# Kernel tuning notes

Hardware: AMD Instinct MI355X
Metric: run time of the kernel (lower is better)

Reference implementation:

```python
import jax, jax.numpy as jnp
import numpy as np

B, W, KD, NC, D, NN, NH, AD, HOPS = 512, 4, 64, 32, 256, 16, 8, 32, 4
DH = D // NH
DFF = 4 * D
P = B * W + B
ROLE_WRITER, ROLE_QUERY = 0, 1


def setup_inputs() -> dict:
    key = jax.random.key(0)
    ks = iter(jax.random.split(key, 40))
    f = lambda shape, s=0.02: jax.random.normal(next(ks), shape, dtype=jnp.float32) * s
    inp = {
        'query_keys': jax.random.normal(next(ks), (B, KD), dtype=jnp.float32),
        'writer_keys': jax.random.normal(next(ks), (B, W, KD), dtype=jnp.float32),
        'key_proj_w': f((KD, D)), 'key_proj_b': jnp.zeros((D,), jnp.float32),
        'class_embed': f((NC, D)), 'role_embed': f((3, D)), 'start_node_embed': f((NN, D)),
        'input_ln_g': jnp.ones((D,), jnp.float32), 'input_ln_b': jnp.zeros((D,), jnp.float32),
        'ln1_g': jnp.ones((NN, D), jnp.float32), 'ln1_b': jnp.zeros((NN, D), jnp.float32),
        'wqkv': f((NN, D, 3 * D)), 'bqkv': jnp.zeros((NN, 3 * D), jnp.float32),
        'wo': f((NN, D, D)), 'bo': jnp.zeros((NN, D), jnp.float32),
        'ln2_g': jnp.ones((NN, D), jnp.float32), 'ln2_b': jnp.zeros((NN, D), jnp.float32),
        'w_fc1': f((NN, D, DFF)), 'b_fc1': jnp.zeros((NN, DFF), jnp.float32),
        'w_fc2': f((NN, DFF, D)), 'b_fc2': jnp.zeros((NN, D), jnp.float32),
        'delta_w': jnp.zeros((D, D), jnp.float32), 'delta_b': jnp.zeros((D,), jnp.float32),
        'dir_w': f((D, D)), 'dir_b': jnp.zeros((D,), jnp.float32),
        'mag_w': f((D, 1)), 'mag_b': jnp.full((1,), 2.5, jnp.float32),
        'out_w': f((D, NC)), 'out_b': jnp.zeros((NC,), jnp.float32),
        'address_table': jax.random.normal(next(ks), (NN, AD), dtype=jnp.float32),
        'query_start_nodes': jax.random.randint(next(ks), (B,), 0, NN),
        'writer_labels': jax.random.randint(next(ks), (B, W), 0, NC),
        'writer_start_nodes': jax.random.randint(next(ks), (B, W), 0, NN),
    }
    return inp


def _ln(x):
    m = jnp.mean(x, -1, keepdims=True)
    v = jnp.var(x, -1, keepdims=True)
    return (x - m) * jax.lax.rsqrt(v + 1e-5)


def _forward(query_keys, writer_keys, key_proj_w, key_proj_b, class_embed, role_embed,
             start_node_embed, input_ln_g, input_ln_b, ln1_g, ln1_b, wqkv, bqkv, wo, bo,
             ln2_g, ln2_b, w_fc1, b_fc1, w_fc2, b_fc2, delta_w, delta_b, dir_w, dir_b,
             mag_w, mag_b, out_w, out_b, address_table,
             query_start_nodes, writer_labels, writer_start_nodes):
    # ---- encode writers (encode_writers) ----
    fk = writer_keys.reshape(-1, KD)          # [B*W, KD]
    fl = writer_labels.reshape(-1)            # [B*W]
    fs = writer_start_nodes.reshape(-1)       # [B*W]
    learned_w = fk @ key_proj_w + key_proj_b + class_embed[fl] + start_node_embed[fs] + role_embed[ROLE_WRITER]
    sw = jnp.zeros_like(learned_w).at[:, :KD].set(fk)
    sw = sw.at[:, KD:KD + NC].set(jax.nn.one_hot(fl, NC, dtype=learned_w.dtype))
    enc_w = _ln(learned_w) * input_ln_g + input_ln_b + sw
    # ---- encode queries (encode_queries) ----
    learned_q = query_keys @ key_proj_w + key_proj_b + start_node_embed[query_start_nodes] + role_embed[ROLE_QUERY]
    sq = jnp.zeros_like(learned_q).at[:, :KD].set(query_keys)
    enc_q = _ln(learned_q) * input_ln_g + input_ln_b + sq

    h = jnp.concatenate([enc_w, enc_q], axis=0)          # [P, D]
    node = jnp.concatenate([fs, query_start_nodes], 0)   # [P] current compute node per packet

    inv_sqrt_dh = 1.0 / np.sqrt(DH).astype(np.float32)
    for _ in range(HOPS):
        oh = jax.nn.one_hot(node, NN, dtype=h.dtype)      # [P, NN] dispatch weights

        def pnl(x, Wn, bn):
            # per-node linear: gather-compute-scatter via MoE-style dense dispatch
            xe = jnp.einsum('pn,pd->npd', oh, x)          # [NN, P, din]
            ye = jnp.einsum('npd,ndf->npf', xe, Wn)       # [NN, P, dout]
            return jnp.einsum('npf,pn->pf', ye, oh) + oh @ bn

        # ComputeNodeCell: pre-LN attention among packets at the same node
        x = _ln(h) * (oh @ ln1_g) + oh @ ln1_b
        qkv = pnl(x, wqkv, bqkv)                          # [P, 3D]
        q, k, v = jnp.split(qkv, 3, axis=-1)
        q = q.reshape(P, NH, DH); k = k.reshape(P, NH, DH); v = v.reshape(P, NH, DH)
        scores = jnp.einsum('phd,qhd->hpq', q, k) * inv_sqrt_dh   # [NH, P, P]
        same = node[:, None] == node[None, :]
        scores = jnp.where(same[None], scores, -1e9)
        attn = jax.nn.softmax(scores, axis=-1)
        ao = jnp.einsum('hpq,qhd->phd', attn, v).reshape(P, D)
        h = h + pnl(ao, wo, bo)
        # MLP block
        x2 = _ln(h) * (oh @ ln2_g) + oh @ ln2_b
        h = h + pnl(jax.nn.gelu(pnl(x2, w_fc1, b_fc1)), w_fc2, b_fc2)
        # routing heads: pick next node from address table, apply gated delta
        direction = h @ dir_w + dir_b
        node = jnp.argmax(direction[:, :AD] @ address_table.T, axis=-1)
        h = h + (h @ delta_w + delta_b) * jax.nn.sigmoid(h @ mag_w + mag_b)

    return h @ out_w + out_b                              # [P, NC] per-packet logits


def reference(query_keys, writer_keys, key_proj_w, key_proj_b, class_embed, role_embed,
              start_node_embed, input_ln_g, input_ln_b, ln1_g, ln1_b, wqkv, bqkv, wo, bo,
              ln2_g, ln2_b, w_fc1, b_fc1, w_fc2, b_fc2, delta_w, delta_b, dir_w, dir_b,
              mag_w, mag_b, out_w, out_b, address_table,
              query_start_nodes, writer_labels, writer_start_nodes):
    return _forward(query_keys, writer_keys, key_proj_w, key_proj_b, class_embed, role_embed,
                    start_node_embed, input_ln_g, input_ln_b, ln1_g, ln1_b, wqkv, bqkv, wo, bo,
                    ln2_g, ln2_b, w_fc1, b_fc1, w_fc2, b_fc2, delta_w, delta_b, dir_w, dir_b,
                    mag_w, mag_b, out_w, out_b, address_table,
                    query_start_nodes, writer_labels, writer_start_nodes)
```

## Files before the change

kernel.cpp:

```cpp
#include <hip/hip_runtime.h>
#include <math.h>

#define B_    512
#define W_    4
#define KD_   64
#define NC_   32
#define D_    256
#define NN_   16
#define NH_   8
#define AD_   32
#define HOPS_ 4
#define DH_   32
#define DFF_  1024
#define P_    2560
#define BW_   2048
#define MAXT_ 56

#define INV_SQRT_DH 0.17677669529663687f

__device__ __forceinline__ float block_sum256(float v, float* red) {
#pragma unroll
  for (int off = 32; off > 0; off >>= 1) v += __shfl_xor(v, off, 64);
  int wid = threadIdx.x >> 6;
  if ((threadIdx.x & 63) == 0) red[wid] = v;
  __syncthreads();
  float s = red[0] + red[1] + red[2] + red[3];
  __syncthreads();
  return s;
}

__device__ __forceinline__ float gelu_tanh(float v) {
  float u = 0.7978845608028654f * (v + 0.044715f * v * v * v);
  return 0.5f * v * (1.0f + tanhf(u));
}

__global__ __launch_bounds__(256) void encode_kernel(
    const float* __restrict__ query_keys, const float* __restrict__ writer_keys,
    const float* __restrict__ kpw, const float* __restrict__ kpb,
    const float* __restrict__ ce, const float* __restrict__ re,
    const float* __restrict__ sne, const float* __restrict__ ilg,
    const float* __restrict__ ilb, const int* __restrict__ qsn,
    const int* __restrict__ wl, const int* __restrict__ wsn,
    float* __restrict__ h, int* __restrict__ node) {
  int p = blockIdx.x, t = threadIdx.x;
  __shared__ float fk[KD_];
  __shared__ float red[4];
  const float* key;
  int lab = -1, sn, role;
  if (p < BW_) { key = writer_keys + (size_t)p * KD_; lab = wl[p]; sn = wsn[p]; role = 0; }
  else { int b = p - BW_; key = query_keys + (size_t)b * KD_; sn = qsn[b]; role = 1; }
  if (t < KD_) fk[t] = key[t];
  __syncthreads();

  float acc = kpb[t] + sne[sn * D_ + t] + re[role * D_ + t];
  if (lab >= 0) acc += ce[lab * D_ + t];
#pragma unroll 8
  for (int i = 0; i < KD_; i++) acc += fk[i] * kpw[i * D_ + t];

  float mean = block_sum256(acc, red) * (1.0f / D_);
  float d = acc - mean;
  float var = block_sum256(d * d, red) * (1.0f / D_);
  float xn = d * (1.0f / sqrtf(var + 1e-5f));

  float sw = 0.0f;
  if (t < KD_) sw = fk[t];
  else if (lab >= 0 && t < KD_ + NC_) sw = (t - KD_ == lab) ? 1.0f : 0.0f;

  h[(size_t)p * D_ + t] = xn * ilg[t] + ilb[t] + sw;
  if (t == 0) node[p] = sn;
}

__global__ __launch_bounds__(256) void sort_kernel(const int* __restrict__ node,
                                                   int* __restrict__ order,
                                                   int* __restrict__ invord,
                                                   int* __restrict__ offs,
                                                   int* __restrict__ cnts,
                                                   int* __restrict__ tnode,
                                                   int* __restrict__ tstart,
                                                   int* __restrict__ tend,
                                                   int* __restrict__ ntiles) {
  __shared__ int c[NN_], o[NN_], cur[NN_];
  int t = threadIdx.x;
  if (t < NN_) c[t] = 0;
  __syncthreads();
  for (int p = t; p < P_; p += 256) atomicAdd(&c[node[p]], 1);
  __syncthreads();
  if (t == 0) {
    int s = 0;
    for (int n = 0; n < NN_; n++) { o[n] = s; cur[n] = s; s += c[n]; }
    int idx = 0;
    for (int n = 0; n < NN_; n++) {
      int e = o[n] + c[n];
      for (int m0 = o[n]; m0 < e; m0 += 64) {
        tnode[idx] = n; tstart[idx] = m0; tend[idx] = e; idx++;
      }
    }
    ntiles[0] = idx;
  }
  __syncthreads();
  if (t < NN_) { cnts[t] = c[t]; offs[t] = o[t]; }
  for (int p = t; p < P_; p += 256) {
    int r = atomicAdd(&cur[node[p]], 1);
    order[r] = p;
    invord[p] = r;
  }
}

__global__ __launch_bounds__(256) void ln_affine(const float* __restrict__ h,
                                                 const float* __restrict__ g,
                                                 const float* __restrict__ b,
                                                 const int* __restrict__ node,
                                                 const int* __restrict__ order,
                                                 float* __restrict__ x) {
  int sp = blockIdx.x, t = threadIdx.x;
  __shared__ float red[4];
  int p = order[sp];
  int n = node[p];
  float v = h[(size_t)p * D_ + t];
  float mean = block_sum256(v, red) * (1.0f / D_);
  float d = v - mean;
  float var = block_sum256(d * d, red) * (1.0f / D_);
  float xn = d * (1.0f / sqrtf(var + 1e-5f));
  x[(size_t)sp * D_ + t] = xn * g[n * D_ + t] + b[n * D_ + t];
}

template <int DIN, int DOUT, int JT, int ACT, int RESID, int PER_NODE, int KSPLIT, int ADDP>
__global__ __launch_bounds__(256) void glin(const float* __restrict__ x,
                                            const float* __restrict__ W,
                                            const float* __restrict__ bias,
                                            float* __restrict__ out,
                                            float* __restrict__ pbuf,
                                            const int* __restrict__ order,
                                            const int* __restrict__ invord,
                                            const int* __restrict__ tnode,
                                            const int* __restrict__ tstart,
                                            const int* __restrict__ tend,
                                            const int* __restrict__ ntiles) {
  constexpr int KC = 32, STX = 68;
  constexpr int CPT = JT / 16;
  constexpr int HALF = 64;
  constexpr int KLEN = DIN / KSPLIT;
  constexpr int NCH = KLEN / KC;
  constexpr int LPR = JT / 4;
  constexpr int RPI = 64 / LPR;

  int ti = blockIdx.x;
  int n, s0, s1;
  if (PER_NODE) {
    if (ti >= ntiles[0]) return;
    n = tnode[ti]; s0 = tstart[ti]; s1 = tend[ti];
  } else {
    n = 0; s0 = ti * 64; s1 = P_;
  }
  int jbase = blockIdx.y * JT;
  int kz = (KSPLIT > 1) ? blockIdx.z : 0;
  int k0 = kz * KLEN;
  int rows = s1 - s0; if (rows > 64) rows = 64;

  __shared__ float xs[2][KC][STX];
  __shared__ float ws[2][KC][JT];

  int tid = threadIdx.x;
  const float* Wn = W + (size_t)n * DIN * DOUT + jbase;

  int xrow = tid >> 2, xq = tid & 3;
  bool xvalid = xrow < rows;
  const float* xptr = x + (size_t)(s0 + (xvalid ? xrow : 0)) * DIN + k0 + xq * 4;
  const float* pptr = nullptr;
  if (ADDP) {
    int pr = xvalid ? invord[s0 + xrow] : 0;
    pptr = pbuf + (size_t)pr * DIN + k0 + xq * 4;
  }

  float4 xr0, xr1;
  auto xfetch = [&](int kc) {
    if (xvalid) {
      xr0 = *(const float4*)(xptr + kc);
      xr1 = *(const float4*)(xptr + kc + 16);
      if (ADDP) {
        float4 p0 = *(const float4*)(pptr + kc);
        float4 p1 = *(const float4*)(pptr + kc + 16);
        xr0.x += p0.x; xr0.y += p0.y; xr0.z += p0.z; xr0.w += p0.w;
        xr1.x += p1.x; xr1.y += p1.y; xr1.z += p1.z; xr1.w += p1.w;
      }
    } else {
      xr0 = make_float4(0.f, 0.f, 0.f, 0.f);
      xr1 = make_float4(0.f, 0.f, 0.f, 0.f);
    }
  };
  auto xstage = [&](int buf) {
    xs[buf][xq * 4 + 0][xrow] = xr0.x;
    xs[buf][xq * 4 + 1][xrow] = xr0.y;
    xs[buf][xq * 4 + 2][xrow] = xr0.z;
    xs[buf][xq * 4 + 3][xrow] = xr0.w;
    xs[buf][xq * 4 + 16][xrow] = xr1.x;
    xs[buf][xq * 4 + 17][xrow] = xr1.y;
    xs[buf][xq * 4 + 18][xrow] = xr1.z;
    xs[buf][xq * 4 + 19][xrow] = xr1.w;
  };
  int wvw = tid >> 6, lane = tid & 63;
  int wlr = lane / LPR;
  int wlc = (lane % LPR) * 4;
  auto wfetch = [&](int buf, int kc) {
#pragma unroll
    for (int i = 0; i < 8 / RPI; i++) {
      int kr = wvw * 8 + i * RPI;
      const float* g = &Wn[(size_t)(k0 + kc + kr + wlr) * DOUT + wlc];
      __builtin_amdgcn_global_load_lds(
          (const __attribute__((address_space(1))) unsigned int*)g,
          (__attribute__((address_space(3))) unsigned int*)&ws[buf][kr][0],
          16, 0, 0);
    }
  };

  wfetch(0, 0);
  xfetch(0);
  xstage(0);
  __syncthreads();

  int r4 = (tid >> 4) * 4;
  int jc4 = (tid & 15) * 4;
  float acc[4][CPT];
#pragma unroll
  for (int r = 0; r < 4; r++)
#pragma unroll
    for (int cc = 0; cc < CPT; cc++) acc[r][cc] = 0.f;

  for (int c = 0; c < NCH; c++) {
    int cur = c & 1;
    if (c + 1 < NCH) {
      wfetch(cur ^ 1, (c + 1) * KC);
      xfetch((c + 1) * KC);
    }
#pragma unroll 8
    for (int k = 0; k < KC; k++) {
      float4 a = *(const float4*)&xs[cur][k][r4];
      float av[4] = {a.x, a.y, a.z, a.w};
      float bv[CPT];
      float4 b0 = *(const float4*)&ws[cur][k][jc4];
      bv[0] = b0.x; bv[1] = b0.y; bv[2] = b0.z; bv[3] = b0.w;
      if (CPT == 8) {
        float4 b1 = *(const float4*)&ws[cur][k][jc4 + HALF];
        bv[4] = b1.x; bv[5] = b1.y; bv[6] = b1.z; bv[7] = b1.w;
      }
#pragma unroll
      for (int r = 0; r < 4; r++)
#pragma unroll
        for (int cc = 0; cc < CPT; cc++) acc[r][cc] += av[r] * bv[cc];
    }
    if (c + 1 < NCH) xstage(cur ^ 1);
    __syncthreads();
  }

  bool main_part = (KSPLIT == 1) || (kz == 0);
  float bbv[CPT];
#pragma unroll
  for (int cc = 0; cc < 4; cc++) bbv[cc] = bias[n * DOUT + jbase + jc4 + cc];
  if (CPT == 8) {
#pragma unroll
    for (int cc = 0; cc < 4; cc++) bbv[4 + cc] = bias[n * DOUT + jbase + jc4 + HALF + cc];
  }

#pragma unroll
  for (int r = 0; r < 4; r++) {
    int lr = r4 + r;
    if (lr >= rows) continue;
    float v[CPT];
    if (main_part) {
#pragma unroll
      for (int cc = 0; cc < CPT; cc++) {
        v[cc] = acc[r][cc] + bbv[cc];
        if (ACT == 1) v[cc] = gelu_tanh(v[cc]);
      }
      if (RESID) {
        int pp = PER_NODE ? order[s0 + lr] : (s0 + lr);
        float* op = &out[(size_t)pp * DOUT + jbase + jc4];
        {
          float4 old = *(const float4*)op;
          *(float4*)op = make_float4(v[0] + old.x, v[1] + old.y, v[2] + old.z, v[3] + old.w);
        }
        if (CPT == 8) {
          float4 old = *(const float4*)(op + HALF);
          *(float4*)(op + HALF) =
              make_float4(v[4] + old.x, v[5] + old.y, v[6] + old.z, v[7] + old.w);
        }
      } else {
        float* op = &out[(size_t)(s0 + lr) * DOUT + jbase + jc4];
        *(float4*)op = make_float4(v[0], v[1], v[2], v[3]);
        if (CPT == 8)
          *(float4*)(op + HALF) = make_float4(v[4], v[5], v[6], v[7]);
      }
    } else {
      float* op = &pbuf[(size_t)(s0 + lr) * DOUT + jbase + jc4];
      *(float4*)op = make_float4(acc[r][0], acc[r][1], acc[r][2], acc[r][3]);
      if (CPT == 8)
        *(float4*)(op + HALF) = make_float4(acc[r][4], acc[r][5], acc[r][6], acc[r][7]);
    }
  }
}

#define ATS 36
__global__ __launch_bounds__(256) void attn_kernel(const float* __restrict__ qkv,
                                                   const int* __restrict__ node,
                                                   const int* __restrict__ order,
                                                   const int* __restrict__ offs,
                                                   const int* __restrict__ cnts,
                                                   float* __restrict__ ao) {
  __shared__ float qs[32 * ATS];
  __shared__ float kts[32 * ATS];
  __shared__ float vs[32 * ATS];
  __shared__ float ps[32 * ATS];
  __shared__ int glo[32], ghi[32];

  int t = threadIdx.x;
  int r = t >> 3;
  int j4 = (t & 7) * 4;
  int r0 = blockIdx.x * 32;
  int hd = blockIdx.y;

  if (t < 32) {
    int n = node[order[r0 + t]];
    glo[t] = offs[n];
    ghi[t] = offs[n] + cnts[n];
  }
  __syncthreads();

  {
    const float* qp = &qkv[(size_t)(r0 + r) * 768 + hd * 32 + j4];
    float4 q4 = *(const float4*)qp;
    q4.x *= INV_SQRT_DH; q4.y *= INV_SQRT_DH; q4.z *= INV_SQRT_DH; q4.w *= INV_SQRT_DH;
    *(float4*)&qs[r * ATS + j4] = q4;
  }

  int lo = glo[0];
  int hi = ghi[31];
  int myglo = glo[r], myghi = ghi[r];

  float4 o4 = {0.f, 0.f, 0.f, 0.f};
  float mrow = -1e30f, lrow = 0.f;

  for (int kt = lo; kt < hi; kt += 32) {
    int sj = kt + r;
    float4 k4 = {0.f, 0.f, 0.f, 0.f}, v4 = {0.f, 0.f, 0.f, 0.f};
    if (sj < hi) {
      const float* kp = &qkv[(size_t)sj * 768 + 256 + hd * 32 + j4];
      k4 = *(const float4*)kp;
      v4 = *(const float4*)(kp + 256);
    }
    __syncthreads();
    kts[(j4 + 0) * ATS + r] = k4.x;
    kts[(j4 + 1) * ATS + r] = k4.y;
    kts[(j4 + 2) * ATS + r] = k4.z;
    kts[(j4 + 3) * ATS + r] = k4.w;
    *(float4*)&vs[r * ATS + j4] = v4;
    __syncthreads();

    float s0 = 0.f, s1 = 0.f, s2 = 0.f, s3 = 0.f;
#pragma unroll 8
    for (int d = 0; d < 32; d++) {
      float qv = qs[r * ATS + d];
      float4 kv = *(const float4*)&kts[d * ATS + j4];
      s0 += qv * kv.x; s1 += qv * kv.y; s2 += qv * kv.z; s3 += qv * kv.w;
    }
    int c0 = kt + j4;
    if (c0 + 0 < myglo || c0 + 0 >= myghi) s0 = -1e30f;
    if (c0 + 1 < myglo || c0 + 1 >= myghi) s1 = -1e30f;
    if (c0 + 2 < myglo || c0 + 2 >= myghi) s2 = -1e30f;
    if (c0 + 3 < myglo || c0 + 3 >= myghi) s3 = -1e30f;

    float mx = fmaxf(fmaxf(s0, s1), fmaxf(s2, s3));
#pragma unroll
    for (int off = 4; off > 0; off >>= 1) mx = fmaxf(mx, __shfl_xor(mx, off, 8));
    float mnew = fmaxf(mrow, mx);
    float alpha = __expf(mrow - mnew);
    float p0 = __expf(s0 - mnew), p1 = __expf(s1 - mnew);
    float p2 = __expf(s2 - mnew), p3 = __expf(s3 - mnew);
    float ls = p0 + p1 + p2 + p3;
#pragma unroll
    for (int off = 4; off > 0; off >>= 1) ls += __shfl_xor(ls, off, 8);
    lrow = lrow * alpha + ls;
    mrow = mnew;
    o4.x *= alpha; o4.y *= alpha; o4.z *= alpha; o4.w *= alpha;

    *(float4*)&ps[r * ATS + j4] = make_float4(p0, p1, p2, p3);
#pragma unroll 8
    for (int j = 0; j < 32; j++) {
      float pj = ps[r * ATS + j];
      float4 vv = *(const float4*)&vs[j * ATS + j4];
      o4.x += pj * vv.x; o4.y += pj * vv.y; o4.z += pj * vv.z; o4.w += pj * vv.w;
    }
  }

  float inv = 1.f / lrow;
  o4.x *= inv; o4.y *= inv; o4.z *= inv; o4.w *= inv;
  *(float4*)&ao[(size_t)(r0 + r) * D_ + hd * 32 + j4] = o4;
}

__global__ __launch_bounds__(256) void route_kernel(float* __restrict__ h,
                                                    const float* __restrict__ pbuf,
                                                    const int* __restrict__ invord,
                                                    const float* __restrict__ dir_w,
                                                    const float* __restrict__ dir_b,
                                                    const float* __restrict__ at,
                                                    const float* __restrict__ mag_w,
                                                    const float* __restrict__ mag_b,
                                                    const float* __restrict__ delta,
                                                    int* __restrict__ node) {
  int p = blockIdx.x, t = threadIdx.x;
  __shared__ float hs[D_];
  __shared__ float dpart[8][AD_];
  __shared__ float dirs[AD_];
  __shared__ float scs[NN_];
  __shared__ float red[4];
  float hv = h[(size_t)p * D_ + t] + pbuf[(size_t)invord[p] * D_ + t];
  hs[t] = hv;
  __syncthreads();

  int j = t & 31, seg = t >> 5;
  float part = 0.0f;
#pragma unroll 8
  for (int i = 0; i < 32; i++) {
    int ii = seg * 32 + i;
    part += hs[ii] * dir_w[ii * D_ + j];
  }
  dpart[seg][j] = part;
  __syncthreads();
  if (t < AD_) {
    float s = dir_b[t];
#pragma unroll
    for (int g = 0; g < 8; g++) s += dpart[g][t];
    dirs[t] = s;
  }
  __syncthreads();
  if (t < NN_) {
    float s = 0.0f;
#pragma unroll
    for (int a = 0; a < AD_; a++) s += dirs[a] * at[t * AD_ + a];
    scs[t] = s;
  }
  __syncthreads();
  if (t == 0) {
    float best = scs[0];
    int arg = 0;
    for (int nn = 1; nn < NN_; nn++)
      if (scs[nn] > best) { best = scs[nn]; arg = nn; }
    node[p] = arg;
  }
  float mag = block_sum256(hv * mag_w[t], red) + mag_b[0];
  float sig = 1.0f / (1.0f + __expf(-mag));
  h[(size_t)p * D_ + t] = hv + delta[(size_t)p * D_ + t] * sig;
}

__global__ __launch_bounds__(256) void out_kernel(const float* __restrict__ h,
                                                  const float* __restrict__ ow,
                                                  const float* __restrict__ ob,
                                                  float* __restrict__ out) {
  int p = blockIdx.x, t = threadIdx.x;
  __shared__ float hs[D_];
  __shared__ float part[8][NC_];
  hs[t] = h[(size_t)p * D_ + t];
  __syncthreads();
  int j = t & 31, seg = t >> 5;
  float s = 0.0f;
#pragma unroll 8
  for (int i = 0; i < 32; i++) {
    int ii = seg * 32 + i;
    s += hs[ii] * ow[ii * NC_ + j];
  }
  part[seg][j] = s;
  __syncthreads();
  if (t < NC_) {
    float r = ob[t];
#pragma unroll
    for (int g = 0; g < 8; g++) r += part[g][t];
    out[(size_t)p * NC_ + t] = r;
  }
}

extern "C" void kernel_launch(void* const* d_in, const int* in_sizes, int n_in,
                              void* d_out, int out_size, void* d_ws, size_t ws_size,
                              hipStream_t stream) {
  (void)in_sizes; (void)n_in; (void)out_size; (void)ws_size;
  const float* query_keys       = (const float*)d_in[0];
  const float* writer_keys      = (const float*)d_in[1];
  const float* key_proj_w       = (const float*)d_in[2];
  const float* key_proj_b       = (const float*)d_in[3];
  const float* class_embed      = (const float*)d_in[4];
  const float* role_embed       = (const float*)d_in[5];
  const float* start_node_embed = (const float*)d_in[6];
  const float* input_ln_g       = (const float*)d_in[7];
  const float* input_ln_b       = (const float*)d_in[8];
  const float* ln1_g            = (const float*)d_in[9];
  const float* ln1_b            = (const float*)d_in[10];
  const float* wqkv             = (const float*)d_in[11];
  const float* bqkv             = (const float*)d_in[12];
  const float* wo               = (const float*)d_in[13];
  const float* bo               = (const float*)d_in[14];
  const float* ln2_g            = (const float*)d_in[15];
  const float* ln2_b            = (const float*)d_in[16];
  const float* w_fc1            = (const float*)d_in[17];
  const float* b_fc1            = (const float*)d_in[18];
  const float* w_fc2            = (const float*)d_in[19];
  const float* b_fc2            = (const float*)d_in[20];
  const float* delta_w          = (const float*)d_in[21];
  const float* delta_b          = (const float*)d_in[22];
  const float* dir_w            = (const float*)d_in[23];
  const float* dir_b            = (const float*)d_in[24];
  const float* mag_w            = (const float*)d_in[25];
  const float* mag_b            = (const float*)d_in[26];
  const float* out_w            = (const float*)d_in[27];
  const float* out_b            = (const float*)d_in[28];
  const float* address_table    = (const float*)d_in[29];
  const int* query_start_nodes  = (const int*)d_in[30];
  const int* writer_labels      = (const int*)d_in[31];
  const int* writer_start_nodes = (const int*)d_in[32];

  uintptr_t basep = (uintptr_t)d_ws;
  auto carve = [&](size_t bytes) {
    basep = (basep + 255) & ~(uintptr_t)255;
    void* r = (void*)basep;
    basep += bytes;
    return r;
  };
  float* h    = (float*)carve((size_t)P_ * D_ * 4);
  float* x    = (float*)carve((size_t)P_ * D_ * 4);
  float* qkvb = (float*)carve((size_t)P_ * 3 * D_ * 4);
  float* ff   = (float*)carve((size_t)P_ * DFF_ * 4);
  float* pbuf = (float*)carve((size_t)P_ * D_ * 4);
  int* node   = (int*)carve(P_ * 4);
  int* order  = (int*)carve(P_ * 4);
  int* invord = (int*)carve(P_ * 4);
  int* offs   = (int*)carve(NN_ * 4);
  int* cnts   = (int*)carve(NN_ * 4);
  int* tnode  = (int*)carve(MAXT_ * 4);
  int* tstart = (int*)carve(MAXT_ * 4);
  int* tend   = (int*)carve(MAXT_ * 4);
  int* ntiles = (int*)carve(4);

  encode_kernel<<<P_, 256, 0, stream>>>(query_keys, writer_keys, key_proj_w, key_proj_b,
                                        class_embed, role_embed, start_node_embed,
                                        input_ln_g, input_ln_b, query_start_nodes,
                                        writer_labels, writer_start_nodes, h, node);

  for (int hop = 0; hop < HOPS_; ++hop) {
    sort_kernel<<<1, 256, 0, stream>>>(node, order, invord, offs, cnts,
                                       tnode, tstart, tend, ntiles);
    ln_affine<<<P_, 256, 0, stream>>>(h, ln1_g, ln1_b, node, order, x);
    glin<256, 768, 128, 0, 0, 1, 1, 0><<<dim3(MAXT_, 6), 256, 0, stream>>>(
        x, wqkv, bqkv, qkvb, nullptr, order, invord, tnode, tstart, tend, ntiles);
    attn_kernel<<<dim3(P_ / 32, NH_), 256, 0, stream>>>(qkvb, node, order, offs, cnts,
                                                        x );
    glin<256, 256, 64, 0, 1, 1, 1, 0><<<dim3(MAXT_, 4), 256, 0, stream>>>(
        x, wo, bo, h, nullptr, order, invord, tnode, tstart, tend, ntiles);
    ln_affine<<<P_, 256, 0, stream>>>(h, ln2_g, ln2_b, node, order, x);
    glin<256, 1024, 128, 1, 0, 1, 1, 0><<<dim3(MAXT_, 8), 256, 0, stream>>>(
        x, w_fc1, b_fc1, ff, nullptr, order, invord, tnode, tstart, tend, ntiles);
    glin<1024, 256, 128, 0, 1, 1, 2, 0><<<dim3(MAXT_, 2, 2), 256, 0, stream>>>(
        ff, w_fc2, b_fc2, h, pbuf, order, invord, tnode, tstart, tend, ntiles);
    glin<256, 256, 64, 0, 0, 0, 1, 1><<<dim3(P_ / 64, 4), 256, 0, stream>>>(
        h, delta_w, delta_b, qkvb , pbuf, order, invord,
        tnode, tstart, tend, ntiles);
    route_kernel<<<P_, 256, 0, stream>>>(h, pbuf, invord, dir_w, dir_b, address_table,
                                         mag_w, mag_b, qkvb, node);
  }

  out_kernel<<<P_, 256, 0, stream>>>(h, out_w, out_b, (float*)d_out);
}
```

Before: 962.8 us.

## Split-K the QKV and FC1 GEMMs, folding partial sums into consumers

The QKV and FC1 projections now use a two-way K split, which doubles their grid. The two partial outputs go to separate buffers. Attention sums the two QKV partials when it loads Q/K/V, and the FC2 kernel sums the two FC1 partials and applies GELU in its input fetch. This adds parallelism to under-occupied per-node GEMMs, at the cost of extra partial-buffer traffic and GELU being recomputed per output column tile.

```diff
diff --git a/kernel.cpp b/kernel.cpp
--- a/kernel.cpp
+++ b/kernel.cpp
@@ -124,12 +124,13 @@
   x[(size_t)sp * D_ + t] = xn * g[n * D_ + t] + b[n * D_ + t];
 }
 
-template <int DIN, int DOUT, int JT, int ACT, int RESID, int PER_NODE, int KSPLIT, int ADDP>
+template <int DIN, int DOUT, int JT, int ACT, int RESID, int PER_NODE, int KSPLIT, int XMODE>
 __global__ __launch_bounds__(256) void glin(const float* __restrict__ x,
                                             const float* __restrict__ W,
                                             const float* __restrict__ bias,
                                             float* __restrict__ out,
                                             float* __restrict__ pbuf,
+                                            const float* __restrict__ xaux,
                                             const int* __restrict__ order,
                                             const int* __restrict__ invord,
                                             const int* __restrict__ tnode,
@@ -166,10 +167,12 @@
   int xrow = tid >> 2, xq = tid & 3;
   bool xvalid = xrow < rows;
   const float* xptr = x + (size_t)(s0 + (xvalid ? xrow : 0)) * DIN + k0 + xq * 4;
-  const float* pptr = nullptr;
-  if (ADDP) {
+  const float* aptr = nullptr;
+  if (XMODE == 1) {
     int pr = xvalid ? invord[s0 + xrow] : 0;
-    pptr = pbuf + (size_t)pr * DIN + k0 + xq * 4;
+    aptr = xaux + (size_t)pr * DIN + k0 + xq * 4;
+  } else if (XMODE == 2) {
+    aptr = xaux + (size_t)(s0 + (xvalid ? xrow : 0)) * DIN + k0 + xq * 4;
   }
 
   float4 xr0, xr1;
@@ -177,11 +180,17 @@
     if (xvalid) {
       xr0 = *(const float4*)(xptr + kc);
       xr1 = *(const float4*)(xptr + kc + 16);
-      if (ADDP) {
-        float4 p0 = *(const float4*)(pptr + kc);
-        float4 p1 = *(const float4*)(pptr + kc + 16);
+      if (XMODE != 0) {
+        float4 p0 = *(const float4*)(aptr + kc);
+        float4 p1 = *(const float4*)(aptr + kc + 16);
         xr0.x += p0.x; xr0.y += p0.y; xr0.z += p0.z; xr0.w += p0.w;
         xr1.x += p1.x; xr1.y += p1.y; xr1.z += p1.z; xr1.w += p1.w;
+        if (XMODE == 2) {
+          xr0.x = gelu_tanh(xr0.x); xr0.y = gelu_tanh(xr0.y);
+          xr0.z = gelu_tanh(xr0.z); xr0.w = gelu_tanh(xr0.w);
+          xr1.x = gelu_tanh(xr1.x); xr1.y = gelu_tanh(xr1.y);
+          xr1.z = gelu_tanh(xr1.z); xr1.w = gelu_tanh(xr1.w);
+        }
       }
     } else {
       xr0 = make_float4(0.f, 0.f, 0.f, 0.f);
@@ -301,6 +310,7 @@
 
 #define ATS 36
 __global__ __launch_bounds__(256) void attn_kernel(const float* __restrict__ qkv,
+                                                   const float* __restrict__ qkvp,
                                                    const int* __restrict__ node,
                                                    const int* __restrict__ order,
                                                    const int* __restrict__ offs,
@@ -326,9 +336,13 @@
   __syncthreads();
 
   {
-    const float* qp = &qkv[(size_t)(r0 + r) * 768 + hd * 32 + j4];
-    float4 q4 = *(const float4*)qp;
-    q4.x *= INV_SQRT_DH; q4.y *= INV_SQRT_DH; q4.z *= INV_SQRT_DH; q4.w *= INV_SQRT_DH;
+    size_t off = (size_t)(r0 + r) * 768 + hd * 32 + j4;
+    float4 q4 = *(const float4*)&qkv[off];
+    float4 qp = *(const float4*)&qkvp[off];
+    q4.x = (q4.x + qp.x) * INV_SQRT_DH;
+    q4.y = (q4.y + qp.y) * INV_SQRT_DH;
+    q4.z = (q4.z + qp.z) * INV_SQRT_DH;
+    q4.w = (q4.w + qp.w) * INV_SQRT_DH;
     *(float4*)&qs[r * ATS + j4] = q4;
   }
 
@@ -343,9 +357,13 @@
     int sj = kt + r;
     float4 k4 = {0.f, 0.f, 0.f, 0.f}, v4 = {0.f, 0.f, 0.f, 0.f};
     if (sj < hi) {
-      const float* kp = &qkv[(size_t)sj * 768 + 256 + hd * 32 + j4];
-      k4 = *(const float4*)kp;
-      v4 = *(const float4*)(kp + 256);
+      size_t off = (size_t)sj * 768 + 256 + hd * 32 + j4;
+      k4 = *(const float4*)&qkv[off];
+      float4 kp = *(const float4*)&qkvp[off];
+      k4.x += kp.x; k4.y += kp.y; k4.z += kp.z; k4.w += kp.w;
+      v4 = *(const float4*)&qkv[off + 256];
+      float4 vp = *(const float4*)&qkvp[off + 256];
+      v4.x += vp.x; v4.y += vp.y; v4.z += vp.z; v4.w += vp.w;
     }
     __syncthreads();
     kts[(j4 + 0) * ATS + r] = k4.x;
@@ -524,7 +542,7 @@
   };
   float* h    = (float*)carve((size_t)P_ * D_ * 4);
   float* x    = (float*)carve((size_t)P_ * D_ * 4);
-  float* qkvb = (float*)carve((size_t)P_ * 3 * D_ * 4);
+  float* buf1 = (float*)carve((size_t)P_ * DFF_ * 4);
   float* ff   = (float*)carve((size_t)P_ * DFF_ * 4);
   float* pbuf = (float*)carve((size_t)P_ * D_ * 4);
   int* node   = (int*)carve(P_ * 4);
@@ -546,22 +564,22 @@
     sort_kernel<<<1, 256, 0, stream>>>(node, order, invord, offs, cnts,
                                        tnode, tstart, tend, ntiles);
     ln_affine<<<P_, 256, 0, stream>>>(h, ln1_g, ln1_b, node, order, x);
-    glin<256, 768, 128, 0, 0, 1, 1, 0><<<dim3(MAXT_, 6), 256, 0, stream>>>(
-        x, wqkv, bqkv, qkvb, nullptr, order, invord, tnode, tstart, tend, ntiles);
-    attn_kernel<<<dim3(P_ / 32, NH_), 256, 0, stream>>>(qkvb, node, order, offs, cnts,
-                                                        x );
+    glin<256, 768, 128, 0, 0, 1, 2, 0><<<dim3(MAXT_, 6, 2), 256, 0, stream>>>(
+        x, wqkv, bqkv, buf1, ff, nullptr, order, invord, tnode, tstart, tend, ntiles);
+    attn_kernel<<<dim3(P_ / 32, NH_), 256, 0, stream>>>(buf1, ff, node, order, offs,
+                                                        cnts, x );
     glin<256, 256, 64, 0, 1, 1, 1, 0><<<dim3(MAXT_, 4), 256, 0, stream>>>(
-        x, wo, bo, h, nullptr, order, invord, tnode, tstart, tend, ntiles);
+        x, wo, bo, h, nullptr, nullptr, order, invord, tnode, tstart, tend, ntiles);
     ln_affine<<<P_, 256, 0, stream>>>(h, ln2_g, ln2_b, node, order, x);
-    glin<256, 1024, 128, 1, 0, 1, 1, 0><<<dim3(MAXT_, 8), 256, 0, stream>>>(
-        x, w_fc1, b_fc1, ff, nullptr, order, invord, tnode, tstart, tend, ntiles);
-    glin<1024, 256, 128, 0, 1, 1, 2, 0><<<dim3(MAXT_, 2, 2), 256, 0, stream>>>(
-        ff, w_fc2, b_fc2, h, pbuf, order, invord, tnode, tstart, tend, ntiles);
+    glin<256, 1024, 128, 0, 0, 1, 2, 0><<<dim3(MAXT_, 8, 2), 256, 0, stream>>>(
+        x, w_fc1, b_fc1, ff, buf1, nullptr, order, invord, tnode, tstart, tend, ntiles);
+    glin<1024, 256, 128, 0, 1, 1, 2, 2><<<dim3(MAXT_, 2, 2), 256, 0, stream>>>(
+        ff, w_fc2, b_fc2, h, pbuf, buf1, order, invord, tnode, tstart, tend, ntiles);
     glin<256, 256, 64, 0, 0, 0, 1, 1><<<dim3(P_ / 64, 4), 256, 0, stream>>>(
-        h, delta_w, delta_b, qkvb , pbuf, order, invord,
+        h, delta_w, delta_b, buf1 , nullptr, pbuf, order, invord,
         tnode, tstart, tend, ntiles);
     route_kernel<<<P_, 256, 0, stream>>>(h, pbuf, invord, dir_w, dir_b, address_table,
-                                         mag_w, mag_b, qkvb, node);
+                                         mag_w, mag_b, buf1, node);
   }
 
   out_kernel<<<P_, 256, 0, stream>>>(h, out_w, out_b, (float*)d_out);
```

After: 992.8 us. +3.1%, slower.

## Schedule per-node GEMM tiles through an interleaved fixed-slot worklist with grid-stride blocks

Applied to the files above, without the earlier changes.

The sort kernel now writes per-node tiles into a fixed 640-slot table laid out as node + 16*tile_index, with empty slots marked -1. This replaces the compact tile list and its tile count. Each per-node glin block grid-strides over the slots, skipping empty ones, so one block may process several tiles in sequence. The aim appears to be removing the dependency on a device-side tile count and spreading each node's tiles across blocks. The risk is that nodes with many rows put tiles into slots that land on blocks already holding a tile, which serialises work. Each block also has to scan many empty slots.

```diff
diff --git a/kernel.cpp b/kernel.cpp
--- a/kernel.cpp
+++ b/kernel.cpp
@@ -14,7 +14,8 @@
 #define DFF_  1024
 #define P_    2560
 #define BW_   2048
-#define MAXT_ 56
+#define WL_   640
+#define GX_   56
 
 #define INV_SQRT_DH 0.17677669529663687f
 
@@ -77,25 +78,25 @@
                                                    int* __restrict__ cnts,
                                                    int* __restrict__ tnode,
                                                    int* __restrict__ tstart,
-                                                   int* __restrict__ tend,
-                                                   int* __restrict__ ntiles) {
+                                                   int* __restrict__ tend) {
   __shared__ int c[NN_], o[NN_], cur[NN_];
   int t = threadIdx.x;
   if (t < NN_) c[t] = 0;
+  for (int w = t; w < WL_; w += 256) tstart[w] = -1;
   __syncthreads();
   for (int p = t; p < P_; p += 256) atomicAdd(&c[node[p]], 1);
   __syncthreads();
   if (t == 0) {
     int s = 0;
     for (int n = 0; n < NN_; n++) { o[n] = s; cur[n] = s; s += c[n]; }
-    int idx = 0;
     for (int n = 0; n < NN_; n++) {
       int e = o[n] + c[n];
-      for (int m0 = o[n]; m0 < e; m0 += 64) {
-        tnode[idx] = n; tstart[idx] = m0; tend[idx] = e; idx++;
+      int ti = 0;
+      for (int m0 = o[n]; m0 < e; m0 += 64, ti++) {
+        int pos = n + 16 * ti;
+        tnode[pos] = n; tstart[pos] = m0; tend[pos] = e;
       }
     }
-    ntiles[0] = idx;
   }
   __syncthreads();
   if (t < NN_) { cnts[t] = c[t]; offs[t] = o[t]; }
@@ -124,18 +125,18 @@
   x[(size_t)sp * D_ + t] = xn * g[n * D_ + t] + b[n * D_ + t];
 }
 
-template <int DIN, int DOUT, int JT, int ACT, int RESID, int PER_NODE, int KSPLIT, int ADDP>
+template <int DIN, int DOUT, int JT, int ACT, int RESID, int PER_NODE, int KSPLIT, int XMODE>
 __global__ __launch_bounds__(256) void glin(const float* __restrict__ x,
                                             const float* __restrict__ W,
                                             const float* __restrict__ bias,
                                             float* __restrict__ out,
                                             float* __restrict__ pbuf,
+                                            const float* __restrict__ xaux,
                                             const int* __restrict__ order,
                                             const int* __restrict__ invord,
                                             const int* __restrict__ tnode,
                                             const int* __restrict__ tstart,
-                                            const int* __restrict__ tend,
-                                            const int* __restrict__ ntiles) {
+                                            const int* __restrict__ tend) {
   constexpr int KC = 32, STX = 68;
   constexpr int CPT = JT / 16;
   constexpr int HALF = 64;
@@ -144,158 +145,163 @@
   constexpr int LPR = JT / 4;
   constexpr int RPI = 64 / LPR;
 
-  int ti = blockIdx.x;
-  int n, s0, s1;
-  if (PER_NODE) {
-    if (ti >= ntiles[0]) return;
-    n = tnode[ti]; s0 = tstart[ti]; s1 = tend[ti];
-  } else {
-    n = 0; s0 = ti * 64; s1 = P_;
-  }
+  __shared__ float xs[2][KC][STX];
+  __shared__ float ws[2][KC][JT];
+
+  int tid = threadIdx.x;
   int jbase = blockIdx.y * JT;
   int kz = (KSPLIT > 1) ? blockIdx.z : 0;
   int k0 = kz * KLEN;
-  int rows = s1 - s0; if (rows > 64) rows = 64;
-
-  __shared__ float xs[2][KC][STX];
-  __shared__ float ws[2][KC][JT];
-
-  int tid = threadIdx.x;
-  const float* Wn = W + (size_t)n * DIN * DOUT + jbase;
-
-  int xrow = tid >> 2, xq = tid & 3;
-  bool xvalid = xrow < rows;
-  const float* xptr = x + (size_t)(s0 + (xvalid ? xrow : 0)) * DIN + k0 + xq * 4;
-  const float* pptr = nullptr;
-  if (ADDP) {
-    int pr = xvalid ? invord[s0 + xrow] : 0;
-    pptr = pbuf + (size_t)pr * DIN + k0 + xq * 4;
-  }
-
-  float4 xr0, xr1;
-  auto xfetch = [&](int kc) {
-    if (xvalid) {
-      xr0 = *(const float4*)(xptr + kc);
-      xr1 = *(const float4*)(xptr + kc + 16);
-      if (ADDP) {
-        float4 p0 = *(const float4*)(pptr + kc);
-        float4 p1 = *(const float4*)(pptr + kc + 16);
-        xr0.x += p0.x; xr0.y += p0.y; xr0.z += p0.z; xr0.w += p0.w;
-        xr1.x += p1.x; xr1.y += p1.y; xr1.z += p1.z; xr1.w += p1.w;
-      }
+
+  for (int w = blockIdx.x;; w += GX_) {
+    int n, s0, s1;
+    if (PER_NODE) {
+      if (w >= WL_) return;
+      s0 = tstart[w];
+      if (s0 < 0) continue;
+      n = tnode[w]; s1 = tend[w];
     } else {
-      xr0 = make_float4(0.f, 0.f, 0.f, 0.f);
-      xr1 = make_float4(0.f, 0.f, 0.f, 0.f);
-    }
-  };
-  auto xstage = [&](int buf) {
-    xs[buf][xq * 4 + 0][xrow] = xr0.x;
-    xs[buf][xq * 4 + 1][xrow] = xr0.y;
-    xs[buf][xq * 4 + 2][xrow] = xr0.z;
-    xs[buf][xq * 4 + 3][xrow] = xr0.w;
-    xs[buf][xq * 4 + 16][xrow] = xr1.x;
-    xs[buf][xq * 4 + 17][xrow] = xr1.y;
-    xs[buf][xq * 4 + 18][xrow] = xr1.z;
-    xs[buf][xq * 4 + 19][xrow] = xr1.w;
-  };
-  int wvw = tid >> 6, lane = tid & 63;
-  int wlr = lane / LPR;
-  int wlc = (lane % LPR) * 4;
-  auto wfetch = [&](int buf, int kc) {
-#pragma unroll
-    for (int i = 0; i < 8 / RPI; i++) {
-      int kr = wvw * 8 + i * RPI;
-      const float* g = &Wn[(size_t)(k0 + kc + kr + wlr) * DOUT + wlc];
-      __builtin_amdgcn_global_load_lds(
-          (const __attribute__((address_space(1))) unsigned int*)g,
-          (__attribute__((address_space(3))) unsigned int*)&ws[buf][kr][0],
-          16, 0, 0);
-    }
-  };
-
-  wfetch(0, 0);
-  xfetch(0);
-  xstage(0);
-  __syncthreads();
-
-  int r4 = (tid >> 4) * 4;
-  int jc4 = (tid & 15) * 4;
-  float acc[4][CPT];
-#pragma unroll
-  for (int r = 0; r < 4; r++)
-#pragma unroll
-    for (int cc = 0; cc < CPT; cc++) acc[r][cc] = 0.f;
-
-  for (int c = 0; c < NCH; c++) {
-    int cur = c & 1;
-    if (c + 1 < NCH) {
-      wfetch(cur ^ 1, (c + 1) * KC);
-      xfetch((c + 1) * KC);
-    }
-#pragma unroll 8
-    for (int k = 0; k < KC; k++) {
-      float4 a = *(const float4*)&xs[cur][k][r4];
-      float av[4] = {a.x, a.y, a.z, a.w};
-      float bv[CPT];
-      float4 b0 = *(const float4*)&ws[cur][k][jc4];
-      bv[0] = b0.x; bv[1] = b0.y; bv[2] = b0.z; bv[3] = b0.w;
-      if (CPT == 8) {
-        float4 b1 = *(const float4*)&ws[cur][k][jc4 + HALF];
-        bv[4] = b1.x; bv[5] = b1.y; bv[6] = b1.z; bv[7] = b1.w;
-      }
-#pragma unroll
-      for (int r = 0; r < 4; r++)
-#pragma unroll
-        for (int cc = 0; cc < CPT; cc++) acc[r][cc] += av[r] * bv[cc];
-    }
-    if (c + 1 < NCH) xstage(cur ^ 1);
-    __syncthreads();
-  }
-
-  bool main_part = (KSPLIT == 1) || (kz == 0);
-  float bbv[CPT];
-#pragma unroll
-  for (int cc = 0; cc < 4; cc++) bbv[cc] = bias[n * DOUT + jbase + jc4 + cc];
-  if (CPT == 8) {
-#pragma unroll
-    for (int cc = 0; cc < 4; cc++) bbv[4 + cc] = bias[n * DOUT + jbase + jc4 + HALF + cc];
-  }
-
-#pragma unroll
-  for (int r = 0; r < 4; r++) {
-    int lr = r4 + r;
-    if (lr >= rows) continue;
-    float v[CPT];
-    if (main_part) {
-#pragma unroll
-      for (int cc = 0; cc < CPT; cc++) {
-        v[cc] = acc[r][cc] + bbv[cc];
-        if (ACT == 1) v[cc] = gelu_tanh(v[cc]);
-      }
-      if (RESID) {
-        int pp = PER_NODE ? order[s0 + lr] : (s0 + lr);
-        float* op = &out[(size_t)pp * DOUT + jbase + jc4];
-        {
-          float4 old = *(const float4*)op;
-          *(float4*)op = make_float4(v[0] + old.x, v[1] + old.y, v[2] + old.z, v[3] + old.w);
-        }
-        if (CPT == 8) {
-          float4 old = *(const float4*)(op + HALF);
-          *(float4*)(op + HALF) =
-              make_float4(v[4] + old.x, v[5] + old.y, v[6] + old.z, v[7] + old.w);
+      n = 0; s0 = blockIdx.x * 64; s1 = P_;
+    }
+    int rows = s1 - s0; if (rows > 64) rows = 64;
+
+    const float* Wn = W + (size_t)n * DIN * DOUT + jbase;
+
+    int xrow = tid >> 2, xq = tid & 3;
+    bool xvalid = xrow < rows;
+    const float* xptr = x + (size_t)(s0 + (xvalid ? xrow : 0)) * DIN + k0 + xq * 4;
+    const float* aptr = nullptr;
+    if (XMODE == 1) {
+      int pr = xvalid ? invord[s0 + xrow] : 0;
+      aptr = xaux + (size_t)pr * DIN + k0 + xq * 4;
+    }
+
+    float4 xr0, xr1;
+    auto xfetch = [&](int kc) {
+      if (xvalid) {
+        xr0 = *(const float4*)(xptr + kc);
+        xr1 = *(const float4*)(xptr + kc + 16);
+        if (XMODE == 1) {
+          float4 p0 = *(const float4*)(aptr + kc);
+          float4 p1 = *(const float4*)(aptr + kc + 16);
+          xr0.x += p0.x; xr0.y += p0.y; xr0.z += p0.z; xr0.w += p0.w;
+          xr1.x += p1.x; xr1.y += p1.y; xr1.z += p1.z; xr1.w += p1.w;
         }
       } else {
-        float* op = &out[(size_t)(s0 + lr) * DOUT + jbase + jc4];
-        *(float4*)op = make_float4(v[0], v[1], v[2], v[3]);
+        xr0 = make_float4(0.f, 0.f, 0.f, 0.f);
+        xr1 = make_float4(0.f, 0.f, 0.f, 0.f);
+      }
+    };
+    auto xstage = [&](int buf) {
+      xs[buf][xq * 4 + 0][xrow] = xr0.x;
+      xs[buf][xq * 4 + 1][xrow] = xr0.y;
+      xs[buf][xq * 4 + 2][xrow] = xr0.z;
+      xs[buf][xq * 4 + 3][xrow] = xr0.w;
+      xs[buf][xq * 4 + 16][xrow] = xr1.x;
+      xs[buf][xq * 4 + 17][xrow] = xr1.y;
+      xs[buf][xq * 4 + 18][xrow] = xr1.z;
+      xs[buf][xq * 4 + 19][xrow] = xr1.w;
+    };
+    int wvw = tid >> 6, lane = tid & 63;
+    int wlr = lane / LPR;
+    int wlc = (lane % LPR) * 4;
+    auto wfetch = [&](int buf, int kc) {
+#pragma unroll
+      for (int i = 0; i < 8 / RPI; i++) {
+        int kr = wvw * 8 + i * RPI;
+        const float* g = &Wn[(size_t)(k0 + kc + kr + wlr) * DOUT + wlc];
+        __builtin_amdgcn_global_load_lds(
+            (const __attribute__((address_space(1))) unsigned int*)g,
+            (__attribute__((address_space(3))) unsigned int*)&ws[buf][kr][0],
+            16, 0, 0);
+      }
+    };
+
+    wfetch(0, 0);
+    xfetch(0);
+    xstage(0);
+    __syncthreads();
+
+    int r4 = (tid >> 4) * 4;
+    int jc4 = (tid & 15) * 4;
+    float acc[4][CPT];
+#pragma unroll
+    for (int r = 0; r < 4; r++)
+#pragma unroll
+      for (int cc = 0; cc < CPT; cc++) acc[r][cc] = 0.f;
+
+    for (int c = 0; c < NCH; c++) {
+      int cur = c & 1;
+      if (c + 1 < NCH) {
+        wfetch(cur ^ 1, (c + 1) * KC);
+        xfetch((c + 1) * KC);
+      }
+#pragma unroll 8
+      for (int k = 0; k < KC; k++) {
+        float4 a = *(const float4*)&xs[cur][k][r4];
+        float av[4] = {a.x, a.y, a.z, a.w};
+        float bv[CPT];
+        float4 b0 = *(const float4*)&ws[cur][k][jc4];
+        bv[0] = b0.x; bv[1] = b0.y; bv[2] = b0.z; bv[3] = b0.w;
+        if (CPT == 8) {
+          float4 b1 = *(const float4*)&ws[cur][k][jc4 + HALF];
+          bv[4] = b1.x; bv[5] = b1.y; bv[6] = b1.z; bv[7] = b1.w;
+        }
+#pragma unroll
+        for (int r = 0; r < 4; r++)
+#pragma unroll
+          for (int cc = 0; cc < CPT; cc++) acc[r][cc] += av[r] * bv[cc];
+      }
+      if (c + 1 < NCH) xstage(cur ^ 1);
+      __syncthreads();
+    }
+
+    bool main_part = (KSPLIT == 1) || (kz == 0);
+    float bbv[CPT];
+#pragma unroll
+    for (int cc = 0; cc < 4; cc++) bbv[cc] = bias[n * DOUT + jbase + jc4 + cc];
+    if (CPT == 8) {
+#pragma unroll
+      for (int cc = 0; cc < 4; cc++) bbv[4 + cc] = bias[n * DOUT + jbase + jc4 + HALF + cc];
+    }
+
+#pragma unroll
+    for (int r = 0; r < 4; r++) {
+      int lr = r4 + r;
+      if (lr >= rows) continue;
+      float v[CPT];
+      if (main_part) {
+#pragma unroll
+        for (int cc = 0; cc < CPT; cc++) {
+          v[cc] = acc[r][cc] + bbv[cc];
+          if (ACT == 1) v[cc] = gelu_tanh(v[cc]);
+        }
+        if (RESID) {
+          int pp = PER_NODE ? order[s0 + lr] : (s0 + lr);
+          float* op = &out[(size_t)pp * DOUT + jbase + jc4];
+          {
+            float4 old = *(const float4*)op;
+            *(float4*)op = make_float4(v[0] + old.x, v[1] + old.y, v[2] + old.z, v[3] + old.w);
+          }
+          if (CPT == 8) {
+            float4 old = *(const float4*)(op + HALF);
+            *(float4*)(op + HALF) =
+                make_float4(v[4] + old.x, v[5] + old.y, v[6] + old.z, v[7] + old.w);
+          }
+        } else {
+          float* op = &out[(size_t)(s0 + lr) * DOUT + jbase + jc4];
+          *(float4*)op = make_float4(v[0], v[1], v[2], v[3]);
+          if (CPT == 8)
+            *(float4*)(op + HALF) = make_float4(v[4], v[5], v[6], v[7]);
+        }
+      } else {
+        float* op = &pbuf[(size_t)(s0 + lr) * DOUT + jbase + jc4];
+        *(float4*)op = make_float4(acc[r][0], acc[r][1], acc[r][2], acc[r][3]);
         if (CPT == 8)
-          *(float4*)(op + HALF) = make_float4(v[4], v[5], v[6], v[7]);
+          *(float4*)(op + HALF) = make_float4(acc[r][4], acc[r][5], acc[r][6], acc[r][7]);
       }
-    } else {
-      float* op = &pbuf[(size_t)(s0 + lr) * DOUT + jbase + jc4];
-      *(float4*)op = make_float4(acc[r][0], acc[r][1], acc[r][2], acc[r][3]);
-      if (CPT == 8)
-        *(float4*)(op + HALF) = make_float4(acc[r][4], acc[r][5], acc[r][6], acc[r][7]);
-    }
+    }
+    if (!PER_NODE) return;
   }
 }
 
@@ -524,7 +530,7 @@
   };
   float* h    = (float*)carve((size_t)P_ * D_ * 4);
   float* x    = (float*)carve((size_t)P_ * D_ * 4);
-  float* qkvb = (float*)carve((size_t)P_ * 3 * D_ * 4);
+  float* buf1 = (float*)carve((size_t)P_ * DFF_ * 4);
   float* ff   = (float*)carve((size_t)P_ * DFF_ * 4);
   float* pbuf = (float*)carve((size_t)P_ * D_ * 4);
   int* node   = (int*)carve(P_ * 4);
@@ -532,10 +538,9 @@
   int* invord = (int*)carve(P_ * 4);
   int* offs   = (int*)carve(NN_ * 4);
   int* cnts   = (int*)carve(NN_ * 4);
-  int* tnode  = (int*)carve(MAXT_ * 4);
-  int* tstart = (int*)carve(MAXT_ * 4);
-  int* tend   = (int*)carve(MAXT_ * 4);
-  int* ntiles = (int*)carve(4);
+  int* tnode  = (int*)carve(WL_ * 4);
+  int* tstart = (int*)carve(WL_ * 4);
+  int* tend   = (int*)carve(WL_ * 4);
 
   encode_kernel<<<P_, 256, 0, stream>>>(query_keys, writer_keys, key_proj_w, key_proj_b,
                                         class_embed, role_embed, start_node_embed,
@@ -544,24 +549,24 @@
 
   for (int hop = 0; hop < HOPS_; ++hop) {
     sort_kernel<<<1, 256, 0, stream>>>(node, order, invord, offs, cnts,
-                                       tnode, tstart, tend, ntiles);
+                                       tnode, tstart, tend);
     ln_affine<<<P_, 256, 0, stream>>>(h, ln1_g, ln1_b, node, order, x);
-    glin<256, 768, 128, 0, 0, 1, 1, 0><<<dim3(MAXT_, 6), 256, 0, stream>>>(
-        x, wqkv, bqkv, qkvb, nullptr, order, invord, tnode, tstart, tend, ntiles);
-    attn_kernel<<<dim3(P_ / 32, NH_), 256, 0, stream>>>(qkvb, node, order, offs, cnts,
-                                                        x );
-    glin<256, 256, 64, 0, 1, 1, 1, 0><<<dim3(MAXT_, 4), 256, 0, stream>>>(
-        x, wo, bo, h, nullptr, order, invord, tnode, tstart, tend, ntiles);
+    glin<256, 768, 128, 0, 0, 1, 1, 0><<<dim3(GX_, 6), 256, 0, stream>>>(
+        x, wqkv, bqkv, buf1, nullptr, nullptr, order, invord, tnode, tstart, tend);
+    attn_kernel<<<dim3(P_ / 32, NH_), 256, 0, stream>>>(buf1, node, order, offs,
+                                                        cnts, x );
+    glin<256, 256, 64, 0, 1, 1, 1, 0><<<dim3(GX_, 4), 256, 0, stream>>>(
+        x, wo, bo, h, nullptr, nullptr, order, invord, tnode, tstart, tend);
     ln_affine<<<P_, 256, 0, stream>>>(h, ln2_g, ln2_b, node, order, x);
-    glin<256, 1024, 128, 1, 0, 1, 1, 0><<<dim3(MAXT_, 8), 256, 0, stream>>>(
-        x, w_fc1, b_fc1, ff, nullptr, order, invord, tnode, tstart, tend, ntiles);
-    glin<1024, 256, 128, 0, 1, 1, 2, 0><<<dim3(MAXT_, 2, 2), 256, 0, stream>>>(
-        ff, w_fc2, b_fc2, h, pbuf, order, invord, tnode, tstart, tend, ntiles);
+    glin<256, 1024, 128, 1, 0, 1, 1, 0><<<dim3(GX_, 8), 256, 0, stream>>>(
+        x, w_fc1, b_fc1, ff, nullptr, nullptr, order, invord, tnode, tstart, tend);
+    glin<1024, 256, 128, 0, 1, 1, 2, 0><<<dim3(GX_, 2, 2), 256, 0, stream>>>(
+        ff, w_fc2, b_fc2, h, pbuf, nullptr, order, invord, tnode, tstart, tend);
     glin<256, 256, 64, 0, 0, 0, 1, 1><<<dim3(P_ / 64, 4), 256, 0, stream>>>(
-        h, delta_w, delta_b, qkvb , pbuf, order, invord,
-        tnode, tstart, tend, ntiles);
+        h, delta_w, delta_b, buf1 , nullptr, pbuf, order, invord,
+        tnode, tstart, tend);
     route_kernel<<<P_, 256, 0, stream>>>(h, pbuf, invord, dir_w, dir_b, address_table,
-                                         mag_w, mag_b, qkvb, node);
+                                         mag_w, mag_b, buf1, node);
   }
 
   out_kernel<<<P_, 256, 0, stream>>>(h, out_w, out_b, (float*)d_out);
```

Measured after the change: 1.480 ms. 53.8% more time.
